# Kernel optimization log

Measured on AMD Instinct MI355X. Metric: run time of the kernel, lower is better.

## Reference

```python
import jax, jax.numpy as jnp
import numpy as np

N = 33554432
NUM_CLASSES = 1000


def setup_inputs() -> dict:
    key = jax.random.key(0)
    k1, k2, k3 = jax.random.split(key, 3)
    confidences = jax.random.uniform(k1, (N,), dtype=jnp.float32)  # max-prob in [0,1)
    predictions = jax.random.randint(k2, (N,), 0, NUM_CLASSES, dtype=jnp.int64)
    labels = jax.random.randint(k3, (N,), 0, NUM_CLASSES, dtype=jnp.int64)
    return {"confidences": confidences, "predictions": predictions,
            "labels": labels, "n_bins": 10}


def reference(confidences, predictions, labels, n_bins):
    # Bin i covers (i/n_bins, (i+1)/n_bins]; conf == 0.0 goes to bin 0 (matches torch loop).
    n = confidences.shape[0]
    boundaries = jnp.linspace(0.0, 1.0, n_bins + 1, dtype=confidences.dtype)
    # searchsorted over upper boundaries: first upper >= conf -> bin index
    bins = jnp.searchsorted(boundaries[1:], confidences, side="left")
    bins = jnp.clip(bins, 0, n_bins - 1)

    acc = (predictions == labels).astype(confidences.dtype)
    ones = jnp.ones_like(confidences)

    cnt = jax.ops.segment_sum(ones, bins, num_segments=n_bins)
    acc_sum = jax.ops.segment_sum(acc, bins, num_segments=n_bins)
    conf_sum = jax.ops.segment_sum(confidences, bins, num_segments=n_bins)

    nonempty = cnt > 0
    safe_cnt = jnp.where(nonempty, cnt, jnp.ones_like(cnt))
    gap = jnp.abs(conf_sum / safe_cnt - acc_sum / safe_cnt)
    prop = cnt / n
    ece = jnp.sum(jnp.where(nonempty, gap * prop, jnp.zeros_like(gap)))
    return ece
```

## Files before the change

kernel.cpp:

```cpp
#include <hip/hip_runtime.h>


#define NBLK 2048
#define TPB  256
#define NTH  (NBLK * TPB)
#define MAXB 256

#define SB(J)                                                   \
  { bool g = ((float)(J) * 0.1f) < v;                           \
    c##J += (unsigned)__popcll(__ballot(g));                    \
    a##J += g ? okf : 0.0f;                                     \
    t##J += g ? v : 0.0f; }

#define SLOT(cx, px, lx)                                        \
  { float v = (cx);                                             \
    float okf = ((px) == (lx)) ? 1.0f : 0.0f;                   \
    cAll += (unsigned)__popcll(__ballot(1));                    \
    tAll += v; aAll += okf;                                     \
    SB(1) SB(2) SB(3) SB(4) SB(5) SB(6) SB(7) SB(8) SB(9) }

#define WRED(x)                                                 \
  { x += __shfl_xor(x, 32, 64); x += __shfl_xor(x, 16, 64);     \
    x += __shfl_xor(x, 8, 64);  x += __shfl_xor(x, 4, 64);      \
    x += __shfl_xor(x, 2, 64);  x += __shfl_xor(x, 1, 64); }

__global__ __launch_bounds__(TPB) void ece_partial(
    const float* __restrict__ conf, const int* __restrict__ pred,
    const int* __restrict__ lab, const int* __restrict__ nbins_p,
    int n, int cap,
    float* __restrict__ ws_cnt, float* __restrict__ ws_acc,
    float* __restrict__ ws_conf)
{
  const int nb = nbins_p[0];
  const int tid = blockIdx.x * blockDim.x + threadIdx.x;
  const int lane = threadIdx.x & 63;
  const int wv   = threadIdx.x >> 6;

  __shared__ float l_c[TPB / 64][10];
  __shared__ float l_a[TPB / 64][10];
  __shared__ float l_t[TPB / 64][10];
  __shared__ unsigned g_cnt[MAXB];
  __shared__ unsigned g_acc[MAXB];
  __shared__ float    g_conf[MAXB];

  if (nb == 10 && cap >= 10) {
    unsigned cAll = 0, c1 = 0, c2 = 0, c3 = 0, c4v = 0, c5 = 0, c6 = 0, c7 = 0, c8 = 0, c9 = 0;
    float aAll = 0.f, a1 = 0.f, a2 = 0.f, a3 = 0.f, a4 = 0.f, a5 = 0.f, a6 = 0.f, a7 = 0.f, a8 = 0.f, a9 = 0.f;
    float tAll = 0.f, t1 = 0.f, t2 = 0.f, t3 = 0.f, t4 = 0.f, t5 = 0.f, t6 = 0.f, t7 = 0.f, t8 = 0.f, t9 = 0.f;
#define c4 c4v
    const int n4 = n >> 2;
    const float4* cp4 = (const float4*)conf;
    const int4*   pp4 = (const int4*)pred;
    const int4*   lp4 = (const int4*)lab;

    const int ITERS = (n4 + NTH - 1) / NTH;
    int idx = tid;
    for (int it = 0; it < ITERS; ++it, idx += NTH) {
      if (idx < n4) {
        float4 c = cp4[idx];
        int4   p = pp4[idx];
        int4   l = lp4[idx];
        SLOT(c.x, p.x, l.x)
        SLOT(c.y, p.y, l.y)
        SLOT(c.z, p.z, l.z)
        SLOT(c.w, p.w, l.w)
      }
    }
    if (blockIdx.x == 0 && wv == 0) {
      const int base = n4 << 2;
      if (base < n) {
        int en  = base + lane;
        int enc = en < n ? en : (n - 1);
        float vr = conf[enc];
        int   pr = pred[enc];
        int   lr = lab[enc];
        bool vld = en < n;
        float v   = vld ? vr : 0.0f;
        float okf = (vld && pr == lr) ? 1.0f : 0.0f;
        cAll += (unsigned)__popcll(__ballot(vld));
        tAll += v; aAll += okf;
        SB(1) SB(2) SB(3) SB(4) SB(5) SB(6) SB(7) SB(8) SB(9)
      }
    }
#undef c4

    WRED(aAll) WRED(a1) WRED(a2) WRED(a3) WRED(a4) WRED(a5) WRED(a6) WRED(a7) WRED(a8) WRED(a9)
    WRED(tAll) WRED(t1) WRED(t2) WRED(t3) WRED(t4) WRED(t5) WRED(t6) WRED(t7) WRED(t8) WRED(t9)

    if (lane == 0) {
      l_c[wv][0] = (float)cAll; l_c[wv][1] = (float)c1; l_c[wv][2] = (float)c2;
      l_c[wv][3] = (float)c3;   l_c[wv][4] = (float)c4v; l_c[wv][5] = (float)c5;
      l_c[wv][6] = (float)c6;   l_c[wv][7] = (float)c7; l_c[wv][8] = (float)c8;
      l_c[wv][9] = (float)c9;
      l_a[wv][0] = aAll; l_a[wv][1] = a1; l_a[wv][2] = a2; l_a[wv][3] = a3;
      l_a[wv][4] = a4;   l_a[wv][5] = a5; l_a[wv][6] = a6; l_a[wv][7] = a7;
      l_a[wv][8] = a8;   l_a[wv][9] = a9;
      l_t[wv][0] = tAll; l_t[wv][1] = t1; l_t[wv][2] = t2; l_t[wv][3] = t3;
      l_t[wv][4] = t4;   l_t[wv][5] = t5; l_t[wv][6] = t6; l_t[wv][7] = t7;
      l_t[wv][8] = t8;   l_t[wv][9] = t9;
    }
    __syncthreads();
    if (threadIdx.x < 10) {
      float sc = 0.f, sa = 0.f, st = 0.f;
#pragma unroll
      for (int w = 0; w < TPB / 64; ++w) {
        sc += l_c[w][threadIdx.x];
        sa += l_a[w][threadIdx.x];
        st += l_t[w][threadIdx.x];
      }
      const int o = threadIdx.x * NBLK + blockIdx.x;
      ws_cnt[o]  = sc;
      ws_acc[o]  = sa;
      ws_conf[o] = st;
    }
  } else {
    int nbc = nb < 1 ? 1 : nb;
    if (nbc > MAXB) nbc = MAXB;
    if (nbc > cap) nbc = (cap < 1) ? 1 : cap;
    for (int j = threadIdx.x; j < nbc; j += blockDim.x) { g_cnt[j] = 0u; g_acc[j] = 0u; g_conf[j] = 0.0f; }
    __syncthreads();
    const float delta = 1.0f / (float)nb;
    for (int i = tid; i < n; i += NTH) {
      float v = conf[i];
      int okk = (pred[i] == lab[i]);
      int bin = (int)(v * (float)nb);
      if (bin > nb - 1) bin = nb - 1;
      if (bin < 0) bin = 0;
      while (bin < nb - 1 && (float)(bin + 1) * delta < v) ++bin;
      while (bin > 0 && !((float)bin * delta < v)) --bin;
      if (bin > nbc - 1) bin = nbc - 1;
      atomicAdd(&g_cnt[bin], 1u);
      atomicAdd(&g_acc[bin], (unsigned)okk);
      atomicAdd(&g_conf[bin], v);
    }
    __syncthreads();
    for (int j = threadIdx.x; j < nbc; j += blockDim.x) {
      ws_cnt[j * NBLK + blockIdx.x]  = (float)g_cnt[j];
      ws_acc[j * NBLK + blockIdx.x]  = (float)g_acc[j];
      ws_conf[j * NBLK + blockIdx.x] = g_conf[j];
    }
  }
}

__global__ __launch_bounds__(640) void ece_final(
    const float* __restrict__ ws_cnt, const float* __restrict__ ws_acc,
    const float* __restrict__ ws_conf, const int* __restrict__ nbins_p,
    int n, int cap, float* __restrict__ out)
{
  int nb = nbins_p[0];
  if (nb < 1) nb = 1;
  int mx = cap < MAXB ? cap : MAXB;
  if (nb > mx) nb = mx;
  const int wv   = threadIdx.x >> 6;
  const int lane = threadIdx.x & 63;
  __shared__ double C[MAXB], A[MAXB], T[MAXB];
  for (int j = threadIdx.x; j < MAXB; j += blockDim.x) { C[j] = 0.0; A[j] = 0.0; T[j] = 0.0; }
  __syncthreads();

  const int nrows = (nb == 10) ? 10 : nb;
  for (int row = wv; row < nrows; row += 10) {
    const float4* c4 = (const float4*)(ws_cnt  + (size_t)row * NBLK);
    const float4* a4 = (const float4*)(ws_acc  + (size_t)row * NBLK);
    const float4* t4 = (const float4*)(ws_conf + (size_t)row * NBLK);
    double sc = 0.0, sa = 0.0, st = 0.0;
#pragma unroll
    for (int itr = 0; itr < NBLK / 256; ++itr) {
      float4 a = c4[itr * 64 + lane];
      float4 b = a4[itr * 64 + lane];
      float4 f = t4[itr * 64 + lane];
      sc += ((double)a.x + (double)a.y) + ((double)a.z + (double)a.w);
      sa += ((double)b.x + (double)b.y) + ((double)b.z + (double)b.w);
      st += ((double)f.x + (double)f.y) + ((double)f.z + (double)f.w);
    }
#pragma unroll
    for (int d = 32; d > 0; d >>= 1) {
      sc += __shfl_xor(sc, d, 64);
      sa += __shfl_xor(sa, d, 64);
      st += __shfl_xor(st, d, 64);
    }
    if (lane == 0) { C[row] = sc; A[row] = sa; T[row] = st; }
  }
  __syncthreads();
  if (threadIdx.x == 0) {
    double e = 0.0;
    if (nb == 10) {
      for (int j = 0; j < 10; ++j) {
        double cn = C[j] - (j < 9 ? C[j + 1] : 0.0);
        double ac = A[j] - (j < 9 ? A[j + 1] : 0.0);
        double cf = T[j] - (j < 9 ? T[j + 1] : 0.0);
        if (cn > 0.0) e += fabs(cf / cn - ac / cn) * (cn / (double)n);
      }
    } else {
      for (int j = 0; j < nb; ++j) {
        double cn = C[j];
        if (cn > 0.0) e += fabs(T[j] / cn - A[j] / cn) * (cn / (double)n);
      }
    }
    out[0] = (float)e;
  }
}

extern "C" void kernel_launch(void* const* d_in, const int* in_sizes, int n_in,
                              void* d_out, int out_size, void* d_ws, size_t ws_size,
                              hipStream_t stream) {
  const float* conf = (const float*)d_in[0];
  const int*   pred = (const int*)d_in[1];
  const int*   lab  = (const int*)d_in[2];
  const int*   nbp  = (const int*)d_in[3];
  const int n = in_sizes[0];

  size_t per = ws_size / 3;
  int cap = (int)(per / ((size_t)NBLK * sizeof(float)));
  if (cap > MAXB) cap = MAXB;
  float* ws_cnt  = (float*)d_ws;
  float* ws_acc  = (float*)((char*)d_ws + (size_t)cap * NBLK * sizeof(float));
  float* ws_conf = (float*)((char*)d_ws + 2ull * (size_t)cap * NBLK * sizeof(float));

  ece_partial<<<NBLK, TPB, 0, stream>>>(conf, pred, lab, nbp, n, cap, ws_cnt, ws_acc, ws_conf);
  ece_final<<<1, 640, 0, stream>>>(ws_cnt, ws_acc, ws_conf, nbp, n, cap, (float*)d_out);
}
```

Baseline: 364.3 us.

## Replace cumulative threshold accumulation with per-thread LDS bin histograms

The fast path for 10 bins stops keeping 30 cumulative per-threshold register accumulators updated with ballots. Each element now gets a direct bin index and is added with LDS atomics to a private per-thread histogram (stride 11). Count and correct-count share one packed 16/16 word, and confidence is summed as 24-bit fixed point. The main loop is also unrolled by two, and the final kernel drops the cumulative-difference decode. The gain is much less ALU work per element, paid for with two LDS atomics per element. The fixed-point and 16-bit packed counters could overflow or lose precision with larger per-thread element counts.

```diff
diff --git a/kernel.cpp b/kernel.cpp
--- a/kernel.cpp
+++ b/kernel.cpp
@@ -5,24 +5,10 @@
 #define TPB  256
 #define NTH  (NBLK * TPB)
 #define MAXB 256
-
-#define SB(J)                                                   \
-  { bool g = ((float)(J) * 0.1f) < v;                           \
-    c##J += (unsigned)__popcll(__ballot(g));                    \
-    a##J += g ? okf : 0.0f;                                     \
-    t##J += g ? v : 0.0f; }
-
-#define SLOT(cx, px, lx)                                        \
-  { float v = (cx);                                             \
-    float okf = ((px) == (lx)) ? 1.0f : 0.0f;                   \
-    cAll += (unsigned)__popcll(__ballot(1));                    \
-    tAll += v; aAll += okf;                                     \
-    SB(1) SB(2) SB(3) SB(4) SB(5) SB(6) SB(7) SB(8) SB(9) }
-
-#define WRED(x)                                                 \
-  { x += __shfl_xor(x, 32, 64); x += __shfl_xor(x, 16, 64);     \
-    x += __shfl_xor(x, 8, 64);  x += __shfl_xor(x, 4, 64);      \
-    x += __shfl_xor(x, 2, 64);  x += __shfl_xor(x, 1, 64); }
+#define STR  11
+#define PLANE (TPB * STR)
+#define FIXS 16777216.0f
+#define FIXI (1.0f / 16777216.0f)
 
 __global__ __launch_bounds__(TPB) void ece_partial(
     const float* __restrict__ conf, const int* __restrict__ pred,
@@ -31,73 +17,69 @@
     float* __restrict__ ws_cnt, float* __restrict__ ws_acc,
     float* __restrict__ ws_conf)
 {
-  const int nb = nbins_p[0];
+  __shared__ unsigned sA[PLANE];
+  __shared__ unsigned sB[PLANE];
+  __shared__ float l_c[TPB / 64][10], l_a[TPB / 64][10], l_t[TPB / 64][10];
+
+  const int nb  = nbins_p[0];
   const int tid = blockIdx.x * blockDim.x + threadIdx.x;
-  const int lane = threadIdx.x & 63;
-  const int wv   = threadIdx.x >> 6;
+  const int col = threadIdx.x * STR;
 
-  __shared__ float l_c[TPB / 64][10];
-  __shared__ float l_a[TPB / 64][10];
-  __shared__ float l_t[TPB / 64][10];
-  __shared__ unsigned g_cnt[MAXB];
-  __shared__ unsigned g_acc[MAXB];
-  __shared__ float    g_conf[MAXB];
+#define ELEM(vx, px, lx)                                              \
+  { float v = (vx);                                                   \
+    int ei = (int)(v * 10.0f);                                        \
+    float fe = (float)ei;                                             \
+    int bin = ei + (((fe + 1.0f) * 0.1f < v) ? 1 : 0)                 \
+                 - ((fe * 0.1f < v) ? 0 : 1);                         \
+    bin = bin < 0 ? 0 : (bin > 9 ? 9 : bin);                          \
+    unsigned inc = ((px) == (lx)) ? 0x10001u : 0x10000u;              \
+    atomicAdd(&sA[col + bin], inc);                                   \
+    atomicAdd(&sB[col + bin], (unsigned)(v * FIXS)); }
 
   if (nb == 10 && cap >= 10) {
-    unsigned cAll = 0, c1 = 0, c2 = 0, c3 = 0, c4v = 0, c5 = 0, c6 = 0, c7 = 0, c8 = 0, c9 = 0;
-    float aAll = 0.f, a1 = 0.f, a2 = 0.f, a3 = 0.f, a4 = 0.f, a5 = 0.f, a6 = 0.f, a7 = 0.f, a8 = 0.f, a9 = 0.f;
-    float tAll = 0.f, t1 = 0.f, t2 = 0.f, t3 = 0.f, t4 = 0.f, t5 = 0.f, t6 = 0.f, t7 = 0.f, t8 = 0.f, t9 = 0.f;
-#define c4 c4v
+#pragma unroll
+    for (int j = 0; j < STR; ++j) { sA[col + j] = 0u; sB[col + j] = 0u; }
+
     const int n4 = n >> 2;
     const float4* cp4 = (const float4*)conf;
     const int4*   pp4 = (const int4*)pred;
     const int4*   lp4 = (const int4*)lab;
 
-    const int ITERS = (n4 + NTH - 1) / NTH;
-    int idx = tid;
-    for (int it = 0; it < ITERS; ++it, idx += NTH) {
-      if (idx < n4) {
-        float4 c = cp4[idx];
-        int4   p = pp4[idx];
-        int4   l = lp4[idx];
-        SLOT(c.x, p.x, l.x)
-        SLOT(c.y, p.y, l.y)
-        SLOT(c.z, p.z, l.z)
-        SLOT(c.w, p.w, l.w)
+    const int iters2 = n4 / (2 * NTH);
+    int i = tid;
+    for (int k = 0; k < iters2; ++k, i += 2 * NTH) {
+      float4 c0 = cp4[i];       int4 p0 = pp4[i];       int4 l0 = lp4[i];
+      float4 c1 = cp4[i + NTH]; int4 p1 = pp4[i + NTH]; int4 l1 = lp4[i + NTH];
+      ELEM(c0.x, p0.x, l0.x) ELEM(c0.y, p0.y, l0.y)
+      ELEM(c0.z, p0.z, l0.z) ELEM(c0.w, p0.w, l0.w)
+      ELEM(c1.x, p1.x, l1.x) ELEM(c1.y, p1.y, l1.y)
+      ELEM(c1.z, p1.z, l1.z) ELEM(c1.w, p1.w, l1.w)
+    }
+    for (int r = 2 * NTH * iters2 + tid; r < n4; r += NTH) {
+      float4 c = cp4[r]; int4 p = pp4[r]; int4 l = lp4[r];
+      ELEM(c.x, p.x, l.x) ELEM(c.y, p.y, l.y)
+      ELEM(c.z, p.z, l.z) ELEM(c.w, p.w, l.w)
+    }
+    for (int s = (n4 << 2) + tid; s < n; s += NTH) {
+      ELEM(conf[s], pred[s], lab[s])
+    }
+
+    const int lane = threadIdx.x & 63;
+    const int wv   = threadIdx.x >> 6;
+#pragma unroll
+    for (int j = 0; j < 10; ++j) {
+      unsigned pa = sA[col + j];
+      unsigned qb = sB[col + j];
+      float cc = (float)(pa >> 16);
+      float ac = (float)(pa & 0xFFFFu);
+      float tb = (float)qb * FIXI;
+#pragma unroll
+      for (int d = 32; d > 0; d >>= 1) {
+        cc += __shfl_xor(cc, d, 64);
+        ac += __shfl_xor(ac, d, 64);
+        tb += __shfl_xor(tb, d, 64);
       }
-    }
-    if (blockIdx.x == 0 && wv == 0) {
-      const int base = n4 << 2;
-      if (base < n) {
-        int en  = base + lane;
-        int enc = en < n ? en : (n - 1);
-        float vr = conf[enc];
-        int   pr = pred[enc];
-        int   lr = lab[enc];
-        bool vld = en < n;
-        float v   = vld ? vr : 0.0f;
-        float okf = (vld && pr == lr) ? 1.0f : 0.0f;
-        cAll += (unsigned)__popcll(__ballot(vld));
-        tAll += v; aAll += okf;
-        SB(1) SB(2) SB(3) SB(4) SB(5) SB(6) SB(7) SB(8) SB(9)
-      }
-    }
-#undef c4
-
-    WRED(aAll) WRED(a1) WRED(a2) WRED(a3) WRED(a4) WRED(a5) WRED(a6) WRED(a7) WRED(a8) WRED(a9)
-    WRED(tAll) WRED(t1) WRED(t2) WRED(t3) WRED(t4) WRED(t5) WRED(t6) WRED(t7) WRED(t8) WRED(t9)
-
-    if (lane == 0) {
-      l_c[wv][0] = (float)cAll; l_c[wv][1] = (float)c1; l_c[wv][2] = (float)c2;
-      l_c[wv][3] = (float)c3;   l_c[wv][4] = (float)c4v; l_c[wv][5] = (float)c5;
-      l_c[wv][6] = (float)c6;   l_c[wv][7] = (float)c7; l_c[wv][8] = (float)c8;
-      l_c[wv][9] = (float)c9;
-      l_a[wv][0] = aAll; l_a[wv][1] = a1; l_a[wv][2] = a2; l_a[wv][3] = a3;
-      l_a[wv][4] = a4;   l_a[wv][5] = a5; l_a[wv][6] = a6; l_a[wv][7] = a7;
-      l_a[wv][8] = a8;   l_a[wv][9] = a9;
-      l_t[wv][0] = tAll; l_t[wv][1] = t1; l_t[wv][2] = t2; l_t[wv][3] = t3;
-      l_t[wv][4] = t4;   l_t[wv][5] = t5; l_t[wv][6] = t6; l_t[wv][7] = t7;
-      l_t[wv][8] = t8;   l_t[wv][9] = t9;
+      if (lane == 0) { l_c[wv][j] = cc; l_a[wv][j] = ac; l_t[wv][j] = tb; }
     }
     __syncthreads();
     if (threadIdx.x < 10) {
@@ -114,15 +96,18 @@
       ws_conf[o] = st;
     }
   } else {
+    unsigned* g_cnt = sA;
+    unsigned* g_acc = sA + MAXB;
+    float*    g_conf = (float*)sB;
     int nbc = nb < 1 ? 1 : nb;
     if (nbc > MAXB) nbc = MAXB;
     if (nbc > cap) nbc = (cap < 1) ? 1 : cap;
     for (int j = threadIdx.x; j < nbc; j += blockDim.x) { g_cnt[j] = 0u; g_acc[j] = 0u; g_conf[j] = 0.0f; }
     __syncthreads();
     const float delta = 1.0f / (float)nb;
-    for (int i = tid; i < n; i += NTH) {
-      float v = conf[i];
-      int okk = (pred[i] == lab[i]);
+    for (int i2 = tid; i2 < n; i2 += NTH) {
+      float v = conf[i2];
+      int okk = (pred[i2] == lab[i2]);
       int bin = (int)(v * (float)nb);
       if (bin > nb - 1) bin = nb - 1;
       if (bin < 0) bin = 0;
@@ -140,6 +125,7 @@
       ws_conf[j * NBLK + blockIdx.x] = g_conf[j];
     }
   }
+#undef ELEM
 }
 
 __global__ __launch_bounds__(640) void ece_final(
@@ -157,8 +143,7 @@
   for (int j = threadIdx.x; j < MAXB; j += blockDim.x) { C[j] = 0.0; A[j] = 0.0; T[j] = 0.0; }
   __syncthreads();
 
-  const int nrows = (nb == 10) ? 10 : nb;
-  for (int row = wv; row < nrows; row += 10) {
+  for (int row = wv; row < nb; row += 10) {
     const float4* c4 = (const float4*)(ws_cnt  + (size_t)row * NBLK);
     const float4* a4 = (const float4*)(ws_acc  + (size_t)row * NBLK);
     const float4* t4 = (const float4*)(ws_conf + (size_t)row * NBLK);
@@ -183,18 +168,9 @@
   __syncthreads();
   if (threadIdx.x == 0) {
     double e = 0.0;
-    if (nb == 10) {
-      for (int j = 0; j < 10; ++j) {
-        double cn = C[j] - (j < 9 ? C[j + 1] : 0.0);
-        double ac = A[j] - (j < 9 ? A[j + 1] : 0.0);
-        double cf = T[j] - (j < 9 ? T[j + 1] : 0.0);
-        if (cn > 0.0) e += fabs(cf / cn - ac / cn) * (cn / (double)n);
-      }
-    } else {
-      for (int j = 0; j < nb; ++j) {
-        double cn = C[j];
-        if (cn > 0.0) e += fabs(T[j] / cn - A[j] / cn) * (cn / (double)n);
-      }
+    for (int j = 0; j < nb; ++j) {
+      double cn = C[j];
+      if (cn > 0.0) e += fabs(T[j] / cn - A[j] / cn) * (cn / (double)n);
     }
     out[0] = (float)e;
   }
```

Measured after the change: 364.7 us. Within noise of the previous version (+0.1%).
